# Optimization experiments

Hardware: AMD Instinct MI355X
Metric: run time of the kernel (lower is better)

The kernel has to match this reference:

```python
import jax, jax.numpy as jnp
import numpy as np

NUM_CLASSES = 81
THRESHOLD = 0.5
NEGPOS_RATIO = 3
ALPHA = 1.0
VAR0, VAR1 = 0.1, 0.2  # cfg['variance']
B, P, NOBJ = 64, 8732, 16


def setup_inputs() -> dict:
    key = jax.random.key(0)
    k1, k2, k3, k4, k5, k6, k7 = jax.random.split(key, 7)
    loc_data = jax.random.normal(k1, (B, P, 4), jnp.float32)
    conf_data = jax.random.normal(k2, (B, P, NUM_CLASSES), jnp.float32)
    # priors in center form (cx, cy, w, h), all in (0,1)
    centers = jax.random.uniform(k3, (P, 2), minval=0.05, maxval=0.95)
    sizes = jax.random.uniform(k4, (P, 2), minval=0.05, maxval=0.5)
    priors = jnp.concatenate([centers, sizes], axis=1).astype(jnp.float32)
    # targets: [B, NOBJ, 5] = (x1, y1, x2, y2, label), valid boxes with x1<x2
    tl = jax.random.uniform(k5, (B, NOBJ, 2), maxval=0.6)
    wh = jax.random.uniform(k6, (B, NOBJ, 2), minval=0.05, maxval=0.35)
    labels = jax.random.randint(k7, (B, NOBJ, 1), 0, NUM_CLASSES - 1).astype(jnp.float32)
    targets = jnp.concatenate([tl, tl + wh, labels], axis=2)
    return {"loc_data": loc_data, "conf_data": conf_data, "priors": priors, "targets": targets}


def point_form(boxes):
    # (cx,cy,w,h) -> (x1,y1,x2,y2)
    return jnp.concatenate([boxes[:, :2] - boxes[:, 2:] / 2,
                            boxes[:, :2] + boxes[:, 2:] / 2], axis=1)


def jaccard(a, b):
    # a: [n,4], b: [m,4], point form -> IoU [n,m]
    tl = jnp.maximum(a[:, None, :2], b[None, :, :2])
    br = jnp.minimum(a[:, None, 2:], b[None, :, 2:])
    wh = jnp.clip(br - tl, 0.0)
    inter = wh[..., 0] * wh[..., 1]
    area_a = ((a[:, 2] - a[:, 0]) * (a[:, 3] - a[:, 1]))[:, None]
    area_b = ((b[:, 2] - b[:, 0]) * (b[:, 3] - b[:, 1]))[None, :]
    return inter / (area_a + area_b - inter)


def encode(matched, priors):
    # matched: [P,4] point form GT, priors: [P,4] center form
    g_cxcy = (matched[:, :2] + matched[:, 2:]) / 2 - priors[:, :2]
    g_cxcy = g_cxcy / (VAR0 * priors[:, 2:])
    g_wh = jnp.log((matched[:, 2:] - matched[:, :2]) / priors[:, 2:]) / VAR1
    return jnp.concatenate([g_cxcy, g_wh], axis=1)


def match_one(truths, labels, priors):
    # truths: [NOBJ,4] point form, labels: [NOBJ]
    overlaps = jaccard(truths, point_form(priors))  # [NOBJ, P]
    best_prior_idx = jnp.argmax(overlaps, axis=1)   # [NOBJ]
    best_truth_overlap = jnp.max(overlaps, axis=0)  # [P]
    best_truth_idx = jnp.argmax(overlaps, axis=0)   # [P]
    # ensure every GT keeps its best prior
    best_truth_overlap = best_truth_overlap.at[best_prior_idx].set(2.0)
    best_truth_idx = best_truth_idx.at[best_prior_idx].set(jnp.arange(truths.shape[0]))
    matched = truths[best_truth_idx]                        # [P,4]
    conf = (labels[best_truth_idx] + 1).astype(jnp.int32)   # [P]
    conf = jnp.where(best_truth_overlap < THRESHOLD, 0, conf)
    return encode(matched, priors), conf


def smooth_l1(x):
    ax = jnp.abs(x)
    return jnp.where(ax < 1.0, 0.5 * x * x, ax - 0.5)


def reference(loc_data, conf_data, priors, targets):
    truths = targets[..., :4]
    labels = targets[..., 4]
    loc_t, conf_t = jax.vmap(match_one, in_axes=(0, 0, None))(truths, labels, priors)
    loc_t = jax.lax.stop_gradient(loc_t)  # targets are non-grad in the original
    pos = conf_t > 0                       # [B,P]
    num_pos = pos.sum(axis=1)              # [B]
    # localization loss (smooth L1, sum over positives)
    loss_l = jnp.sum(smooth_l1(loc_data - loc_t) * pos[..., None].astype(loc_data.dtype))
    # per-prior CE = logsumexp(logits) - logit[target]
    lse = jax.nn.logsumexp(conf_data, axis=2)                                   # [B,P]
    gathered = jnp.take_along_axis(conf_data, conf_t[..., None], axis=2)[..., 0]
    loss_c = lse - gathered                                                      # [B,P]
    # hard negative mining: rank negatives by loss, keep top 3*num_pos
    loss_c_mine = jnp.where(pos, 0.0, loss_c)
    idx_rank = jnp.argsort(jnp.argsort(-loss_c_mine, axis=1), axis=1)
    num_neg = jnp.minimum(NEGPOS_RATIO * num_pos, P - 1)
    neg = idx_rank < num_neg[:, None]
    sel = jnp.logical_or(pos, neg)
    loss_conf = jnp.sum(jnp.where(sel, loss_c, 0.0))
    N = num_pos.sum().astype(loc_data.dtype)
    return ALPHA * loss_l / N + loss_conf / N
```

## Files before the change

kernel.cpp:

```cpp
#include <hip/hip_runtime.h>

#define BB 64
#define PP 8732
#define NOBJ 16
#define NC 81
#define THRESH 0.5f
#define NEGPOS 3
#define NCHUNK 4
#define CHUNK (PP / NCHUNK)

#define TK_THREADS 512
#define TK_KEYS 18

__device__ __forceinline__ float smooth_l1(float x) {
    float ax = fabsf(x);
    return (ax < 1.0f) ? 0.5f * x * x : ax - 0.5f;
}

__global__ __launch_bounds__(256) void k_matchA(
    const float* __restrict__ priors, const float* __restrict__ targets,
    unsigned long long* __restrict__ g_best)
{
    const int chunk = blockIdx.x;
    const int b = blockIdx.y;
    const int tid = threadIdx.x;

    __shared__ float s_tx1[NOBJ], s_ty1[NOBJ], s_tx2[NOBJ], s_ty2[NOBJ];
    __shared__ float s_area[NOBJ];
    __shared__ unsigned long long s_best[NOBJ];

    if (tid < NOBJ) {
        const float* t = targets + ((size_t)b * NOBJ + tid) * 5;
        float x1 = t[0], y1 = t[1], x2 = t[2], y2 = t[3];
        s_tx1[tid] = x1; s_ty1[tid] = y1; s_tx2[tid] = x2; s_ty2[tid] = y2;
        s_area[tid] = (x2 - x1) * (y2 - y1);
        s_best[tid] = 0ull;
    }
    __syncthreads();

    unsigned long long best[NOBJ];
    #pragma unroll
    for (int t = 0; t < NOBJ; ++t) best[t] = 0ull;

    const int p0 = chunk * CHUNK, p1 = p0 + CHUNK;
    for (int p = p0 + tid; p < p1; p += 256) {
        float4 pr = ((const float4*)priors)[p];
        float px1 = pr.x - pr.z * 0.5f, py1 = pr.y - pr.w * 0.5f;
        float px2 = pr.x + pr.z * 0.5f, py2 = pr.y + pr.w * 0.5f;
        float pa = (px2 - px1) * (py2 - py1);
        unsigned revp = 0xFFFFFFFFu - (unsigned)p;
        #pragma unroll
        for (int t = 0; t < NOBJ; ++t) {
            float ix1 = fmaxf(s_tx1[t], px1), iy1 = fmaxf(s_ty1[t], py1);
            float ix2 = fminf(s_tx2[t], px2), iy2 = fminf(s_ty2[t], py2);
            float iw = fmaxf(ix2 - ix1, 0.f), ih = fmaxf(iy2 - iy1, 0.f);
            float inter = iw * ih;
            float iou = inter / (s_area[t] + pa - inter);
            unsigned long long key =
                ((unsigned long long)__float_as_uint(iou) << 32) | revp;
            if (key > best[t]) best[t] = key;
        }
    }
    #pragma unroll
    for (int t = 0; t < NOBJ; ++t) {
        unsigned long long v = best[t];
        for (int o = 32; o > 0; o >>= 1) {
            unsigned long long w = __shfl_down(v, o);
            if (w > v) v = w;
        }
        if ((tid & 63) == 0) atomicMax(&s_best[t], v);
    }
    __syncthreads();
    if (tid < NOBJ) atomicMax(&g_best[b * NOBJ + tid], s_best[tid]);
}

__global__ __launch_bounds__(256) void k_matchB(
    const float* __restrict__ loc_data, const float* __restrict__ priors,
    const float* __restrict__ targets, const unsigned long long* __restrict__ g_best,
    unsigned char* __restrict__ conf_t, int* __restrict__ num_pos,
    double* __restrict__ accum)
{
    const int chunk = blockIdx.x;
    const int b = blockIdx.y;
    const int tid = threadIdx.x;

    __shared__ float s_tx1[NOBJ], s_ty1[NOBJ], s_tx2[NOBJ], s_ty2[NOBJ];
    __shared__ float s_lab[NOBJ], s_area[NOBJ];
    __shared__ int s_bpi[NOBJ];

    if (tid < NOBJ) {
        const float* t = targets + ((size_t)b * NOBJ + tid) * 5;
        float x1 = t[0], y1 = t[1], x2 = t[2], y2 = t[3];
        s_tx1[tid] = x1; s_ty1[tid] = y1; s_tx2[tid] = x2; s_ty2[tid] = y2;
        s_lab[tid] = t[4];
        s_area[tid] = (x2 - x1) * (y2 - y1);
        unsigned revp = (unsigned)(g_best[b * NOBJ + tid] & 0xFFFFFFFFull);
        s_bpi[tid] = (int)(0xFFFFFFFFu - revp);
    }
    __syncthreads();

    int n_pos = 0;
    float lloss = 0.f;
    const int p0 = chunk * CHUNK, p1 = p0 + CHUNK;
    for (int p = p0 + tid; p < p1; p += 256) {
        float4 pr = ((const float4*)priors)[p];
        float px1 = pr.x - pr.z * 0.5f, py1 = pr.y - pr.w * 0.5f;
        float px2 = pr.x + pr.z * 0.5f, py2 = pr.y + pr.w * 0.5f;
        float pa = (px2 - px1) * (py2 - py1);
        float bt_ov = -1.f;
        int bt_idx = 0;
        #pragma unroll
        for (int t = 0; t < NOBJ; ++t) {
            float ix1 = fmaxf(s_tx1[t], px1), iy1 = fmaxf(s_ty1[t], py1);
            float ix2 = fminf(s_tx2[t], px2), iy2 = fminf(s_ty2[t], py2);
            float iw = fmaxf(ix2 - ix1, 0.f), ih = fmaxf(iy2 - iy1, 0.f);
            float inter = iw * ih;
            float iou = inter / (s_area[t] + pa - inter);
            if (iou > bt_ov) { bt_ov = iou; bt_idx = t; }
        }
        #pragma unroll
        for (int i = 0; i < NOBJ; ++i)
            if (s_bpi[i] == p) { bt_idx = i; bt_ov = 2.0f; }

        int c = (bt_ov < THRESH) ? 0 : ((int)s_lab[bt_idx] + 1);
        conf_t[(size_t)b * PP + p] = (unsigned char)c;

        if (c > 0) {
            n_pos++;
            float mx1 = s_tx1[bt_idx], my1 = s_ty1[bt_idx];
            float mx2 = s_tx2[bt_idx], my2 = s_ty2[bt_idx];
            float gcx = ((mx1 + mx2) * 0.5f - pr.x) / (0.1f * pr.z);
            float gcy = ((my1 + my2) * 0.5f - pr.y) / (0.1f * pr.w);
            float gw = logf((mx2 - mx1) / pr.z) / 0.2f;
            float gh = logf((my2 - my1) / pr.w) / 0.2f;
            float4 ld = ((const float4*)loc_data)[(size_t)b * PP + p];
            lloss += smooth_l1(ld.x - gcx) + smooth_l1(ld.y - gcy) +
                     smooth_l1(ld.z - gw) + smooth_l1(ld.w - gh);
        }
    }

    for (int o = 32; o > 0; o >>= 1) {
        n_pos += __shfl_down(n_pos, o);
        lloss += __shfl_down(lloss, o);
    }
    __shared__ int s_np[4];
    __shared__ float s_ll[4];
    int wave = tid >> 6, lane = tid & 63;
    if (lane == 0) { s_np[wave] = n_pos; s_ll[wave] = lloss; }
    __syncthreads();
    if (tid == 0) {
        atomicAdd(&num_pos[b], s_np[0] + s_np[1] + s_np[2] + s_np[3]);
        atomicAdd(&accum[0], (double)(s_ll[0] + s_ll[1] + s_ll[2] + s_ll[3]));
    }
}

__global__ __launch_bounds__(256) void k_conf(
    const float* __restrict__ conf_data, const unsigned char* __restrict__ conf_t,
    float* __restrict__ lcm, double* __restrict__ accum)
{
    __shared__ float4 s_buf4[1300];
    float* s_data = (float*)s_buf4;
    const int tid = threadIdx.x;
    const int r = tid >> 2;
    const int s = tid & 3;
    const int seg_start = s * 21;
    const int seg_len = (s == 3) ? 18 : 21;
    const int base_row = blockIdx.x * 256;

    if (tid < 4)
        s_buf4[1296 + tid] = make_float4(-1e30f, -1e30f, -1e30f, -1e30f);

    float posl = 0.f;
    for (int ch = 0; ch < 4; ++ch) {
        const int row0 = base_row + ch * 64;
        const float4* g4 = (const float4*)conf_data + ((size_t)row0 * NC >> 2);
        __syncthreads();
        for (int i = tid; i < 1296; i += 256)
            s_buf4[i] = g4[i];
        __syncthreads();

        const float* myrow = s_data + r * NC;
        float m = -1e30f;
        #pragma unroll
        for (int j = 0; j < 21; ++j) {
            float v = myrow[seg_start + j];
            m = fmaxf(m, (j < seg_len) ? v : -1e30f);
        }
        m = fmaxf(m, __shfl_xor(m, 1));
        m = fmaxf(m, __shfl_xor(m, 2));
        float e = 0.f;
        #pragma unroll
        for (int j = 0; j < 21; ++j) {
            float v = myrow[seg_start + j];
            e += (j < seg_len) ? __expf(v - m) : 0.f;
        }
        e += __shfl_xor(e, 1);
        e += __shfl_xor(e, 2);
        if (s == 0) {
            float lse = m + __logf(e);
            int row = row0 + r;
            int c = (int)conf_t[row];
            float lc = lse - myrow[c];
            bool pos = c > 0;
            lcm[row] = pos ? 0.f : lc;
            if (pos) posl += lc;
        }
    }
    for (int o = 32; o > 0; o >>= 1) posl += __shfl_down(posl, o);
    __shared__ float s_w[4];
    if ((tid & 63) == 0) s_w[tid >> 6] = posl;
    __syncthreads();
    if (tid == 0)
        atomicAdd(&accum[1], (double)(s_w[0] + s_w[1] + s_w[2] + s_w[3]));
}

__global__ __launch_bounds__(TK_THREADS) void k_topk(
    const float* __restrict__ lcm, const int* __restrict__ num_pos,
    double* __restrict__ accum)
{
    const int b = blockIdx.x, tid = threadIdx.x;
    unsigned key[TK_KEYS];
    #pragma unroll
    for (int j = 0; j < TK_KEYS; ++j) {
        int i = tid + j * TK_THREADS;
        key[j] = (i < PP) ? __float_as_uint(lcm[(size_t)b * PP + i]) : 0u;
    }
    __shared__ int s_cnt[32];
    if (tid < 32) s_cnt[tid] = 0;
    int k = NEGPOS * num_pos[b];
    if (k > PP - 1) k = PP - 1;
    __syncthreads();

    unsigned T = 0;
    for (int bit = 30; bit >= 0; --bit) {
        unsigned cand = T | (1u << bit);
        int cnt = 0;
        #pragma unroll
        for (int j = 0; j < TK_KEYS; ++j)
            cnt += (int)__popcll(__ballot(key[j] >= cand));
        if ((tid & 63) == 0) atomicAdd(&s_cnt[bit], cnt);
        __syncthreads();
        if (s_cnt[bit] >= k) T = cand;
    }

    float sum = 0.f;
    int cgt = 0;
    #pragma unroll
    for (int j = 0; j < TK_KEYS; ++j) {
        if (key[j] > T) { sum += __uint_as_float(key[j]); cgt++; }
    }
    for (int o = 32; o > 0; o >>= 1) {
        sum += __shfl_down(sum, o);
        cgt += __shfl_down(cgt, o);
    }
    __shared__ float s_s[8];
    __shared__ int s_c[8];
    if ((tid & 63) == 0) { s_s[tid >> 6] = sum; s_c[tid >> 6] = cgt; }
    __syncthreads();
    if (tid == 0) {
        float tot = 0.f; int ctot = 0;
        for (int w = 0; w < 8; ++w) { tot += s_s[w]; ctot += s_c[w]; }
        float neg = tot + (float)(k - ctot) * __uint_as_float(T);
        atomicAdd(&accum[1], (double)neg);
    }
}

__global__ __launch_bounds__(64) void k_final(
    const int* __restrict__ num_pos, const double* __restrict__ accum,
    float* __restrict__ out)
{
    int tid = threadIdx.x;
    int n = (tid < BB) ? num_pos[tid] : 0;
    for (int o = 32; o > 0; o >>= 1) n += __shfl_down(n, o);
    if (tid == 0)
        out[0] = (float)((accum[0] + accum[1]) / (double)n);
}

extern "C" void kernel_launch(void* const* d_in, const int* in_sizes, int n_in,
                              void* d_out, int out_size, void* d_ws, size_t ws_size,
                              hipStream_t stream) {
    const float* loc_data  = (const float*)d_in[0];
    const float* conf_data = (const float*)d_in[1];
    const float* priors    = (const float*)d_in[2];
    const float* targets   = (const float*)d_in[3];

    char* ws = (char*)d_ws;
    double* accum = (double*)ws;
    int* num_pos = (int*)(ws + 16);
    unsigned long long* g_best = (unsigned long long*)(ws + 512);
    unsigned char* conf_t = (unsigned char*)(ws + 8704);
    float* lcm = (float*)(ws + 8704 + (size_t)BB * PP);

    hipMemsetAsync(ws, 0, 8704, stream);

    dim3 mg(NCHUNK, BB);
    k_matchA<<<mg, 256, 0, stream>>>(priors, targets, g_best);
    k_matchB<<<mg, 256, 0, stream>>>(loc_data, priors, targets, g_best,
                                     conf_t, num_pos, accum);

    k_conf<<<(BB * PP) / 256, 256, 0, stream>>>(conf_data, conf_t, lcm, accum);

    k_topk<<<BB, TK_THREADS, 0, stream>>>(lcm, num_pos, accum);

    k_final<<<1, 64, 0, stream>>>(num_pos, accum, (float*)d_out);
}
```

Measured before the change: 333.6 us.

## Double-buffer conf tiles with register prefetch and fold final reduction into topk

```diff
diff --git a/kernel.cpp b/kernel.cpp
--- a/kernel.cpp
+++ b/kernel.cpp
@@ -158,48 +158,56 @@
     const float* __restrict__ conf_data, const unsigned char* __restrict__ conf_t,
     float* __restrict__ lcm, double* __restrict__ accum)
 {
-    __shared__ float4 s_buf4[1300];
-    float* s_data = (float*)s_buf4;
+    __shared__ float4 s_buf4[2][648];
     const int tid = threadIdx.x;
-    const int r = tid >> 2;
-    const int s = tid & 3;
-    const int seg_start = s * 21;
-    const int seg_len = (s == 3) ? 18 : 21;
+    const int r = tid >> 3;
+    const int s = tid & 7;
+    const int seg_start = s * 10;
+    const int seg_len = (s == 7) ? 11 : 10;
     const int base_row = blockIdx.x * 256;
-
-    if (tid < 4)
-        s_buf4[1296 + tid] = make_float4(-1e30f, -1e30f, -1e30f, -1e30f);
+    const float4* g4base = (const float4*)conf_data;
+
+    float4 t0, t1, t2;
+    {
+        const float4* g4 = g4base + (size_t)base_row * NC / 4;
+        t0 = g4[tid]; t1 = g4[tid + 256];
+        if (tid < 136) t2 = g4[tid + 512];
+    }
 
     float posl = 0.f;
-    for (int ch = 0; ch < 4; ++ch) {
-        const int row0 = base_row + ch * 64;
-        const float4* g4 = (const float4*)conf_data + ((size_t)row0 * NC >> 2);
+    for (int h = 0; h < 8; ++h) {
+        float4* buf = s_buf4[h & 1];
+        buf[tid] = t0; buf[tid + 256] = t1;
+        if (tid < 136) buf[tid + 512] = t2;
+        if (h + 1 < 8) {
+            const float4* g4 = g4base + (size_t)(base_row + (h + 1) * 32) * NC / 4;
+            t0 = g4[tid]; t1 = g4[tid + 256];
+            if (tid < 136) t2 = g4[tid + 512];
+        }
         __syncthreads();
-        for (int i = tid; i < 1296; i += 256)
-            s_buf4[i] = g4[i];
-        __syncthreads();
-
-        const float* myrow = s_data + r * NC;
+
+        const float* myrow = (const float*)buf + r * NC;
+        float v[11];
+        #pragma unroll
+        for (int j = 0; j < 11; ++j) v[j] = myrow[seg_start + j];
+
         float m = -1e30f;
         #pragma unroll
-        for (int j = 0; j < 21; ++j) {
-            float v = myrow[seg_start + j];
-            m = fmaxf(m, (j < seg_len) ? v : -1e30f);
-        }
+        for (int j = 0; j < 11; ++j) m = fmaxf(m, (j < seg_len) ? v[j] : -1e30f);
         m = fmaxf(m, __shfl_xor(m, 1));
         m = fmaxf(m, __shfl_xor(m, 2));
+        m = fmaxf(m, __shfl_xor(m, 4));
         float e = 0.f;
         #pragma unroll
-        for (int j = 0; j < 21; ++j) {
-            float v = myrow[seg_start + j];
-            e += (j < seg_len) ? __expf(v - m) : 0.f;
-        }
+        for (int j = 0; j < 11; ++j) e += (j < seg_len) ? __expf(v[j] - m) : 0.f;
         e += __shfl_xor(e, 1);
         e += __shfl_xor(e, 2);
+        e += __shfl_xor(e, 4);
+
         if (s == 0) {
+            int row = base_row + h * 32 + r;
+            int c = (int)conf_t[row];
             float lse = m + __logf(e);
-            int row = row0 + r;
-            int c = (int)conf_t[row];
             float lc = lse - myrow[c];
             bool pos = c > 0;
             lcm[row] = pos ? 0.f : lc;
@@ -216,7 +224,8 @@
 
 __global__ __launch_bounds__(TK_THREADS) void k_topk(
     const float* __restrict__ lcm, const int* __restrict__ num_pos,
-    double* __restrict__ accum)
+    double* __restrict__ accum, int* __restrict__ done_cnt,
+    float* __restrict__ out)
 {
     const int b = blockIdx.x, tid = threadIdx.x;
     unsigned key[TK_KEYS];
@@ -262,18 +271,16 @@
         for (int w = 0; w < 8; ++w) { tot += s_s[w]; ctot += s_c[w]; }
         float neg = tot + (float)(k - ctot) * __uint_as_float(T);
         atomicAdd(&accum[1], (double)neg);
-    }
-}
-
-__global__ __launch_bounds__(64) void k_final(
-    const int* __restrict__ num_pos, const double* __restrict__ accum,
-    float* __restrict__ out)
-{
-    int tid = threadIdx.x;
-    int n = (tid < BB) ? num_pos[tid] : 0;
-    for (int o = 32; o > 0; o >>= 1) n += __shfl_down(n, o);
-    if (tid == 0)
-        out[0] = (float)((accum[0] + accum[1]) / (double)n);
+        __threadfence();
+        int prev = atomicAdd(done_cnt, 1);
+        if (prev == BB - 1) {
+            double a0 = atomicAdd(&accum[0], 0.0);
+            double a1 = atomicAdd(&accum[1], 0.0);
+            int N = 0;
+            for (int bb = 0; bb < BB; ++bb) N += num_pos[bb];
+            out[0] = (float)((a0 + a1) / (double)N);
+        }
+    }
 }
 
 extern "C" void kernel_launch(void* const* d_in, const int* in_sizes, int n_in,
@@ -286,7 +293,8 @@
 
     char* ws = (char*)d_ws;
     double* accum = (double*)ws;
-    int* num_pos = (int*)(ws + 16);
+    int* done_cnt = (int*)(ws + 16);
+    int* num_pos = (int*)(ws + 32);
     unsigned long long* g_best = (unsigned long long*)(ws + 512);
     unsigned char* conf_t = (unsigned char*)(ws + 8704);
     float* lcm = (float*)(ws + 8704 + (size_t)BB * PP);
@@ -300,7 +308,6 @@
 
     k_conf<<<(BB * PP) / 256, 256, 0, stream>>>(conf_data, conf_t, lcm, accum);
 
-    k_topk<<<BB, TK_THREADS, 0, stream>>>(lcm, num_pos, accum);
-
-    k_final<<<1, 64, 0, stream>>>(num_pos, accum, (float*)d_out);
-}
+    k_topk<<<BB, TK_THREADS, 0, stream>>>(lcm, num_pos, accum, done_cnt,
+                                          (float*)d_out);
+}
```

Result: no change. 327.3 us (-1.9%).
